# Performance work log

Measured on AMD Instinct MI355X. Metric: run time of the kernel, lower is better.

## Reference

```python
import jax, jax.numpy as jnp
import numpy as np

N = 2_000_000
REL_DIM = 14
CAN_DIM = 64
N_TYPES = 4


def setup_inputs() -> dict:
    key = jax.random.key(0)
    ka, kb, kia, kib, kw, kbias = jax.random.split(key, 6)
    return {
        "relation_logits_a": jax.random.normal(ka, (N, REL_DIM), dtype=jnp.float32),
        "relation_logits_b": jax.random.normal(kb, (N, REL_DIM), dtype=jnp.float32),
        "frame_type_ids_a": jax.random.randint(kia, (N,), 0, N_TYPES, dtype=jnp.int32),
        "frame_type_ids_b": jax.random.randint(kib, (N,), 0, N_TYPES, dtype=jnp.int32),
        # stacked expert params: W[e] is (REL_DIM, CAN_DIM), b[e] is (CAN_DIM,)
        "W": jax.random.normal(kw, (N_TYPES, REL_DIM, CAN_DIM), dtype=jnp.float32) * 0.26,
        "b": jax.random.normal(kbias, (N_TYPES, CAN_DIM), dtype=jnp.float32) * 0.26,
    }


def _batch_project(x, ids, W, b):
    # x: (N, REL_DIM), ids: (N,) int in [0, N_TYPES)
    # Masked dispatch to 4 tiny linear experts; peak intermediate is (N, CAN_DIM).
    out = jnp.zeros((x.shape[0], CAN_DIM), dtype=x.dtype)
    for e in range(N_TYPES):
        y = x @ W[e] + b[e]                      # (N, CAN_DIM)
        out = out + jnp.where((ids == e)[:, None], y, jnp.zeros((), x.dtype))
    return out


def reference(relation_logits_a, relation_logits_b, frame_type_ids_a, frame_type_ids_b, W, b):
    proj_a = _batch_project(relation_logits_a, frame_type_ids_a, W, b)
    proj_b = _batch_project(relation_logits_b, frame_type_ids_b, W, b)
    # F.mse_loss default reduction='mean'
    diff = proj_a - proj_b
    return jnp.mean(diff * diff)
```

## Files before the change

### kernel.cpp

```cpp
#include <hip/hip_runtime.h>
#include <hip/hip_bf16.h>
#include <hip/hip_fp16.h>


#define N_ROWS   2000000
#define CHUNK    64
#define N_CHUNKS (N_ROWS / CHUNK)
#define LDSP     72

typedef _Float16       h8  __attribute__((ext_vector_type(8)));
typedef float          f4  __attribute__((ext_vector_type(4)));
typedef unsigned short us8 __attribute__((ext_vector_type(8)));

__device__ __forceinline__ unsigned short f2h_bits(float x) {
    return __builtin_bit_cast(unsigned short, (_Float16)x);
}

__global__ void __launch_bounds__(64)
frame_loss_mfma(const float* __restrict__ A, const float* __restrict__ B,
                const int* __restrict__ IDA, const int* __restrict__ IDB,
                const float* __restrict__ W, const float* __restrict__ BIAS,
                float* __restrict__ out)
{
    __shared__ unsigned short sA[CHUNK * LDSP];
    __shared__ unsigned short sB[CHUNK * LDSP];

    const int lane = threadIdx.x & 63;
    const int sub  = lane & 15;
    const int quad = lane >> 4;

    h8 wf[8], nwf[8];
#pragma unroll
    for (int ct = 0; ct < 4; ++ct) {
#pragma unroll
        for (int s = 0; s < 2; ++s) {
            const int c = ct * 16 + sub;
            us8 bits;
#pragma unroll
            for (int j = 0; j < 8; ++j) {
                const int k = s * 32 + quad * 8 + j;
                float v = 0.0f;
                if (k < 56) {
                    const int e = k / 14;
                    const int kk = k - e * 14;
                    v = W[(e * 14 + kk) * 64 + c];
                } else if (k < 60) {
                    v = BIAS[(k - 56) * 64 + c];
                }
                bits[j] = f2h_bits(v);
            }
            wf[ct * 2 + s] = __builtin_bit_cast(h8, bits);
            us8 nb = bits ^ (unsigned short)0x8000;
            nwf[ct * 2 + s] = __builtin_bit_cast(h8, nb);
        }
    }

    float lsum = 0.0f;
    unsigned int* const rowA32 = (unsigned int*)(sA + lane * LDSP);
    unsigned int* const rowB32 = (unsigned int*)(sB + lane * LDSP);

    for (int chunk = blockIdx.x; chunk < N_CHUNKS; chunk += gridDim.x) {
        const int row = chunk * CHUNK + lane;
        const float2* ap = (const float2*)(A + (size_t)row * 14);
        const float2* bp = (const float2*)(B + (size_t)row * 14);
        float2 av[7], bv[7];
#pragma unroll
        for (int t = 0; t < 7; ++t) av[t] = ap[t];
#pragma unroll
        for (int t = 0; t < 7; ++t) bv[t] = bp[t];
        const int ea = IDA[row];
        const int eb = IDB[row];

        const us8 z = {0, 0, 0, 0, 0, 0, 0, 0};
#pragma unroll
        for (int t = 0; t < 9; ++t) ((us8*)rowA32)[t] = z;
#pragma unroll
        for (int t = 0; t < 9; ++t) ((us8*)rowB32)[t] = z;

#pragma unroll
        for (int t = 0; t < 7; ++t)
            rowA32[7 * ea + t] = (unsigned)f2h_bits(av[t].x) | ((unsigned)f2h_bits(av[t].y) << 16);
        rowA32[28 + (ea >> 1)] = 0x3C00u << (16 * (ea & 1));
#pragma unroll
        for (int t = 0; t < 7; ++t)
            rowB32[7 * eb + t] = (unsigned)f2h_bits(bv[t].x) | ((unsigned)f2h_bits(bv[t].y) << 16);
        rowB32[28 + (eb >> 1)] = 0x3C00u << (16 * (eb & 1));

        __syncthreads();

#pragma unroll
        for (int t = 0; t < 4; ++t) {
            const unsigned short* fa = sA + (t * 16 + sub) * LDSP + quad * 8;
            const unsigned short* fb = sB + (t * 16 + sub) * LDSP + quad * 8;
            h8 a0 = __builtin_bit_cast(h8, *(const us8*)fa);
            h8 a1 = __builtin_bit_cast(h8, *(const us8*)(fa + 32));
            h8 b0 = __builtin_bit_cast(h8, *(const us8*)fb);
            h8 b1 = __builtin_bit_cast(h8, *(const us8*)(fb + 32));
#pragma unroll
            for (int ct = 0; ct < 4; ++ct) {
                f4 acc = {0.0f, 0.0f, 0.0f, 0.0f};
                acc = __builtin_amdgcn_mfma_f32_16x16x32_f16(a0, wf[ct * 2 + 0], acc, 0, 0, 0);
                acc = __builtin_amdgcn_mfma_f32_16x16x32_f16(a1, wf[ct * 2 + 1], acc, 0, 0, 0);
                acc = __builtin_amdgcn_mfma_f32_16x16x32_f16(b0, nwf[ct * 2 + 0], acc, 0, 0, 0);
                acc = __builtin_amdgcn_mfma_f32_16x16x32_f16(b1, nwf[ct * 2 + 1], acc, 0, 0, 0);
                lsum += acc[0] * acc[0] + acc[1] * acc[1] + acc[2] * acc[2] + acc[3] * acc[3];
            }
        }
        __syncthreads();
    }

#pragma unroll
    for (int off = 32; off > 0; off >>= 1)
        lsum += __shfl_down(lsum, off, 64);
    if (lane == 0)
        atomicAdd(out, lsum * (1.0f / 128000000.0f));
}

extern "C" void kernel_launch(void* const* d_in, const int* in_sizes, int n_in,
                              void* d_out, int out_size, void* d_ws, size_t ws_size,
                              hipStream_t stream) {
    const float* A    = (const float*)d_in[0];
    const float* B    = (const float*)d_in[1];
    const int*   IDA  = (const int*)d_in[2];
    const int*   IDB  = (const int*)d_in[3];
    const float* W    = (const float*)d_in[4];
    const float* BIAS = (const float*)d_in[5];
    float* out = (float*)d_out;

    hipMemsetAsync(out, 0, sizeof(float), stream);
    frame_loss_mfma<<<dim3(4096), dim3(64), 0, stream>>>(A, B, IDA, IDB, W, BIAS, out);
}
```

Measured before the change: 280.4 us.

## Compute all four experts per row via MFMA and select results in registers

Replaces the LDS-based one-hot expansion, where the input row is scattered into a 60-wide zero-padded K slot, with direct register fragments. Each wave now runs a 16-row tile through all four experts using the 16x16x16 f16 MFMA and picks each row's expert output with selects on the type id. This drops LDS traffic, zeroing stores and block barriers, and raises the launch to 256-thread blocks of independent waves. In exchange it issues more MFMAs per row and uses uncoalesced per-lane float2 loads from the row-strided input.

New measurement: 335.4 us. +19.6%, slower.

```diff
diff --git a/kernel.cpp b/kernel.cpp
--- a/kernel.cpp
+++ b/kernel.cpp
@@ -1,112 +1,141 @@
 #include <hip/hip_runtime.h>
-#include <hip/hip_bf16.h>
 #include <hip/hip_fp16.h>
 
 
-#define N_ROWS   2000000
-#define CHUNK    64
-#define N_CHUNKS (N_ROWS / CHUNK)
-#define LDSP     72
+#define N_ROWS  2000000
+#define N_TILES (N_ROWS / 16)
 
-typedef _Float16       h8  __attribute__((ext_vector_type(8)));
-typedef float          f4  __attribute__((ext_vector_type(4)));
-typedef unsigned short us8 __attribute__((ext_vector_type(8)));
+typedef _Float16 h4 __attribute__((ext_vector_type(4)));
+typedef _Float16 h8 __attribute__((ext_vector_type(8)));
+typedef float    f4 __attribute__((ext_vector_type(4)));
 
-__device__ __forceinline__ unsigned short f2h_bits(float x) {
-    return __builtin_bit_cast(unsigned short, (_Float16)x);
-}
+#if __has_builtin(__builtin_amdgcn_mfma_f32_16x16x16f16)
+#define USE_K16 1
+#else
+#define USE_K16 0
+#endif
 
-__global__ void __launch_bounds__(64)
-frame_loss_mfma(const float* __restrict__ A, const float* __restrict__ B,
-                const int* __restrict__ IDA, const int* __restrict__ IDB,
-                const float* __restrict__ W, const float* __restrict__ BIAS,
-                float* __restrict__ out)
+__global__ void __launch_bounds__(256)
+frame_loss(const float* __restrict__ A, const float* __restrict__ B,
+           const int* __restrict__ IDA, const int* __restrict__ IDB,
+           const float* __restrict__ W, const float* __restrict__ BIAS,
+           float* __restrict__ out)
 {
-    __shared__ unsigned short sA[CHUNK * LDSP];
-    __shared__ unsigned short sB[CHUNK * LDSP];
-
     const int lane = threadIdx.x & 63;
     const int sub  = lane & 15;
     const int quad = lane >> 4;
+    const int wave   = blockIdx.x * (blockDim.x >> 6) + (threadIdx.x >> 6);
+    const int nwaves = gridDim.x * (blockDim.x >> 6);
 
-    h8 wf[8], nwf[8];
+#if USE_K16
+    h4 wf[16];
 #pragma unroll
-    for (int ct = 0; ct < 4; ++ct) {
+    for (int e = 0; e < 4; ++e)
 #pragma unroll
-        for (int s = 0; s < 2; ++s) {
-            const int c = ct * 16 + sub;
-            us8 bits;
+        for (int g = 0; g < 4; ++g) {
+            h4 f;
+#pragma unroll
+            for (int j = 0; j < 4; ++j) {
+                const int k = quad * 4 + j;
+                const int c = g * 16 + sub;
+                float v = 0.0f;
+                if (k < 14)       v = W[(e * 14 + k) * 64 + c];
+                else if (k == 14) v = BIAS[e * 64 + c];
+                f[j] = (_Float16)v;
+            }
+            wf[e * 4 + g] = f;
+        }
+#else
+    h8 wf[16];
+#pragma unroll
+    for (int e = 0; e < 4; ++e)
+#pragma unroll
+        for (int g = 0; g < 4; ++g) {
+            h8 f;
 #pragma unroll
             for (int j = 0; j < 8; ++j) {
-                const int k = s * 32 + quad * 8 + j;
+                const int k = quad * 8 + j;
+                const int c = g * 16 + sub;
                 float v = 0.0f;
-                if (k < 56) {
-                    const int e = k / 14;
-                    const int kk = k - e * 14;
-                    v = W[(e * 14 + kk) * 64 + c];
-                } else if (k < 60) {
-                    v = BIAS[(k - 56) * 64 + c];
-                }
-                bits[j] = f2h_bits(v);
+                if (k < 14)       v = W[(e * 14 + k) * 64 + c];
+                else if (k == 14) v = BIAS[e * 64 + c];
+                f[j] = (_Float16)v;
             }
-            wf[ct * 2 + s] = __builtin_bit_cast(h8, bits);
-            us8 nb = bits ^ (unsigned short)0x8000;
-            nwf[ct * 2 + s] = __builtin_bit_cast(h8, nb);
+            wf[e * 4 + g] = f;
         }
-    }
+#endif
 
     float lsum = 0.0f;
-    unsigned int* const rowA32 = (unsigned int*)(sA + lane * LDSP);
-    unsigned int* const rowB32 = (unsigned int*)(sB + lane * LDSP);
 
-    for (int chunk = blockIdx.x; chunk < N_CHUNKS; chunk += gridDim.x) {
-        const int row = chunk * CHUNK + lane;
-        const float2* ap = (const float2*)(A + (size_t)row * 14);
-        const float2* bp = (const float2*)(B + (size_t)row * 14);
-        float2 av[7], bv[7];
-#pragma unroll
-        for (int t = 0; t < 7; ++t) av[t] = ap[t];
-#pragma unroll
-        for (int t = 0; t < 7; ++t) bv[t] = bp[t];
-        const int ea = IDA[row];
-        const int eb = IDB[row];
+    for (int t = wave; t < N_TILES; t += nwaves) {
+        const int base = t * 16;
 
-        const us8 z = {0, 0, 0, 0, 0, 0, 0, 0};
-#pragma unroll
-        for (int t = 0; t < 9; ++t) ((us8*)rowA32)[t] = z;
-#pragma unroll
-        for (int t = 0; t < 9; ++t) ((us8*)rowB32)[t] = z;
+        const int4 ia = *(const int4*)(IDA + base + quad * 4);
+        const int4 ib = *(const int4*)(IDB + base + quad * 4);
+        const int* iap = (const int*)&ia;
+        const int* ibp = (const int*)&ib;
+
+        const float2* ra = (const float2*)(A + (size_t)(base + sub) * 14);
+        const float2* rb = (const float2*)(B + (size_t)(base + sub) * 14);
+#if USE_K16
+        float2 a0 = ra[2 * quad];
+        float2 b0 = rb[2 * quad];
+        float2 a1 = (quad < 3) ? ra[2 * quad + 1] : make_float2(1.0f, 0.0f);
+        float2 b1 = (quad < 3) ? rb[2 * quad + 1] : make_float2(1.0f, 0.0f);
+        h4 af, bf;
+        af[0] = (_Float16)a0.x; af[1] = (_Float16)a0.y;
+        af[2] = (_Float16)a1.x; af[3] = (_Float16)a1.y;
+        bf[0] = (_Float16)b0.x; bf[1] = (_Float16)b0.y;
+        bf[2] = (_Float16)b1.x; bf[3] = (_Float16)b1.y;
+#else
+        float2 a0 = {0,0}, a1 = {0,0}, a2 = {0,0}, a3 = {0,0};
+        float2 b0 = {0,0}, b1 = {0,0}, b2 = {0,0}, b3 = {0,0};
+        if (quad == 0) {
+            a0 = ra[0]; a1 = ra[1]; a2 = ra[2]; a3 = ra[3];
+            b0 = rb[0]; b1 = rb[1]; b2 = rb[2]; b3 = rb[3];
+        } else if (quad == 1) {
+            a0 = ra[4]; a1 = ra[5]; a2 = ra[6]; a3 = make_float2(1.0f, 0.0f);
+            b0 = rb[4]; b1 = rb[5]; b2 = rb[6]; b3 = make_float2(1.0f, 0.0f);
+        }
+        h8 af, bf;
+        af[0] = (_Float16)a0.x; af[1] = (_Float16)a0.y;
+        af[2] = (_Float16)a1.x; af[3] = (_Float16)a1.y;
+        af[4] = (_Float16)a2.x; af[5] = (_Float16)a2.y;
+        af[6] = (_Float16)a3.x; af[7] = (_Float16)a3.y;
+        bf[0] = (_Float16)b0.x; bf[1] = (_Float16)b0.y;
+        bf[2] = (_Float16)b1.x; bf[3] = (_Float16)b1.y;
+        bf[4] = (_Float16)b2.x; bf[5] = (_Float16)b2.y;
+        bf[6] = (_Float16)b3.x; bf[7] = (_Float16)b3.y;
+#endif
 
 #pragma unroll
-        for (int t = 0; t < 7; ++t)
-            rowA32[7 * ea + t] = (unsigned)f2h_bits(av[t].x) | ((unsigned)f2h_bits(av[t].y) << 16);
-        rowA32[28 + (ea >> 1)] = 0x3C00u << (16 * (ea & 1));
+        for (int g = 0; g < 4; ++g) {
+            f4 aA[4], aB[4];
+            const f4 z = {0.0f, 0.0f, 0.0f, 0.0f};
 #pragma unroll
-        for (int t = 0; t < 7; ++t)
-            rowB32[7 * eb + t] = (unsigned)f2h_bits(bv[t].x) | ((unsigned)f2h_bits(bv[t].y) << 16);
-        rowB32[28 + (eb >> 1)] = 0x3C00u << (16 * (eb & 1));
-
-        __syncthreads();
-
+            for (int e = 0; e < 4; ++e) {
+#if USE_K16
+                aA[e] = __builtin_amdgcn_mfma_f32_16x16x16f16(af, wf[e * 4 + g], z, 0, 0, 0);
+                aB[e] = __builtin_amdgcn_mfma_f32_16x16x16f16(bf, wf[e * 4 + g], z, 0, 0, 0);
+#else
+                aA[e] = __builtin_amdgcn_mfma_f32_16x16x32_f16(af, wf[e * 4 + g], z, 0, 0, 0);
+                aB[e] = __builtin_amdgcn_mfma_f32_16x16x32_f16(bf, wf[e * 4 + g], z, 0, 0, 0);
+#endif
+            }
 #pragma unroll
-        for (int t = 0; t < 4; ++t) {
-            const unsigned short* fa = sA + (t * 16 + sub) * LDSP + quad * 8;
-            const unsigned short* fb = sB + (t * 16 + sub) * LDSP + quad * 8;
-            h8 a0 = __builtin_bit_cast(h8, *(const us8*)fa);
-            h8 a1 = __builtin_bit_cast(h8, *(const us8*)(fa + 32));
-            h8 b0 = __builtin_bit_cast(h8, *(const us8*)fb);
-            h8 b1 = __builtin_bit_cast(h8, *(const us8*)(fb + 32));
-#pragma unroll
-            for (int ct = 0; ct < 4; ++ct) {
-                f4 acc = {0.0f, 0.0f, 0.0f, 0.0f};
-                acc = __builtin_amdgcn_mfma_f32_16x16x32_f16(a0, wf[ct * 2 + 0], acc, 0, 0, 0);
-                acc = __builtin_amdgcn_mfma_f32_16x16x32_f16(a1, wf[ct * 2 + 1], acc, 0, 0, 0);
-                acc = __builtin_amdgcn_mfma_f32_16x16x32_f16(b0, nwf[ct * 2 + 0], acc, 0, 0, 0);
-                acc = __builtin_amdgcn_mfma_f32_16x16x32_f16(b1, nwf[ct * 2 + 1], acc, 0, 0, 0);
-                lsum += acc[0] * acc[0] + acc[1] * acc[1] + acc[2] * acc[2] + acc[3] * acc[3];
+            for (int r = 0; r < 4; ++r) {
+                const int ja = iap[r];
+                const int jb = ibp[r];
+                float s0 = (ja & 1) ? aA[1][r] : aA[0][r];
+                float s1 = (ja & 1) ? aA[3][r] : aA[2][r];
+                float va = (ja & 2) ? s1 : s0;
+                float t0 = (jb & 1) ? aB[1][r] : aB[0][r];
+                float t1 = (jb & 1) ? aB[3][r] : aB[2][r];
+                float vb = (jb & 2) ? t1 : t0;
+                float d = va - vb;
+                lsum = fmaf(d, d, lsum);
             }
         }
-        __syncthreads();
     }
 
 #pragma unroll
@@ -128,5 +157,5 @@
     float* out = (float*)d_out;
 
     hipMemsetAsync(out, 0, sizeof(float), stream);
-    frame_loss_mfma<<<dim3(4096), dim3(64), 0, stream>>>(A, B, IDA, IDB, W, BIAS, out);
+    frame_loss<<<dim3(2048), dim3(256), 0, stream>>>(A, B, IDA, IDB, W, BIAS, out);
 }
```
